# Optimization experiments

Hardware: AMD Instinct MI355X
Metric: run time of the kernel (lower is better)

Reference implementation:

```python
import jax, jax.numpy as jnp
import numpy as np

C_IN, C_OUT, K, PAD, STRIDE = 128, 256, 3, 1, 1
H = W = 256


def setup_inputs() -> dict:
    key = jax.random.key(0)
    k1, k2, k3 = jax.random.split(key, 3)
    # batch=1: the original forward uses X_pad[0] for every batch index,
    # so with m=1 the buggy loop and a standard conv are mathematically identical.
    x = jax.random.normal(k1, (1, C_IN, H, W), dtype=jnp.float32)
    # nn.Parameter(torch.rand(...)) -> uniform[0,1)
    weight = jax.random.uniform(k2, (C_OUT, C_IN, K, K), dtype=jnp.float32)
    bias = jax.random.uniform(k3, (C_OUT,), dtype=jnp.float32)
    return {"x": x, "weight": weight, "bias": bias}


def reference(x, weight, bias):
    # Faithful math of convAppx.forward with FP_appx_mul treated as exact
    # multiply (FP_appx_mul is not defined in the source): a plain 2D
    # cross-correlation (no kernel flip, matching the sliced elementwise
    # product) with symmetric padding, stride 1, plus per-channel bias.
    z = jax.lax.conv_general_dilated(
        x, weight,
        window_strides=(STRIDE, STRIDE),
        padding=((PAD, PAD), (PAD, PAD)),
        dimension_numbers=("NCHW", "OIHW", "NCHW"),
    )
    return z + bias[None, :, None, None]
```

## Files before the change

kernel.cpp:

```cpp
#include <hip/hip_runtime.h>
#include <hip/hip_bf16.h>


typedef short bf16x8 __attribute__((ext_vector_type(8)));
typedef float f32x4 __attribute__((ext_vector_type(4)));
typedef int   i32x4 __attribute__((ext_vector_type(4)));
typedef unsigned short u16x4 __attribute__((ext_vector_type(4)));
typedef unsigned short u16x8 __attribute__((ext_vector_type(8)));

#define CIN   128
#define COUT  256
#define HH    256
#define WW    256
#define HP    258
#define ROWP  (HP * CIN)

static __device__ __forceinline__ unsigned short f2bf(float v) {
    __hip_bfloat16 b = __float2bfloat16(v);
    return *reinterpret_cast<unsigned short*>(&b);
}

static __device__ __forceinline__ void gload_lds16(const unsigned short* g, unsigned short* l) {
    __builtin_amdgcn_global_load_lds(
        (const __attribute__((address_space(1))) unsigned int*)g,
        (__attribute__((address_space(3))) unsigned int*)l, 16, 0, 0);
}

template<int CTRL>
static __device__ __forceinline__ bf16x8 rotf(bf16x8 a) {
    i32x4 ai = __builtin_bit_cast(i32x4, a);
    i32x4 r;
    #pragma unroll
    for (int j = 0; j < 4; ++j)
        r[j] = __builtin_amdgcn_mov_dpp(ai[j], CTRL, 0xF, 0xF, true);
    return __builtin_bit_cast(bf16x8, r);
}
#define ROR_P1 0x12F
#define ROR_P2 0x12E

__global__ __launch_bounds__(256) void prep_kernel(const float* __restrict__ x,
                                                   const float* __restrict__ w,
                                                   unsigned short* __restrict__ xb,
                                                   unsigned short* __restrict__ wr) {
    int bid = blockIdx.x;
    int t   = threadIdx.x;

    if (bid < 65) {
        int i = bid * 256 + t;
        if (i < 16448) {
            u16x8 z = {0, 0, 0, 0, 0, 0, 0, 0};
            int off;
            if (i < 8256) {
                int r   = (i >= 4128) ? 1 : 0;
                int rem = i - r * 4128;
                off = (r * 257) * ROWP + rem * 8;
            } else {
                int j   = i - 8256;
                int col = j >> 12;
                int rem = j & 4095;
                int hp  = (rem >> 4) + 1;
                int c8  = rem & 15;
                off = hp * ROWP + (col * 257) * CIN + c8 * 8;
            }
            *(u16x8*)(&xb[off]) = z;
        }
    }

    if (bid < 128) {
        int p = bid * 256 + t;
        const float* src = w + p * 9;
        #pragma unroll
        for (int khw = 0; khw < 9; ++khw)
            wr[khw * (COUT * CIN) + p] = f2bf(src[khw]);
    }

    int h  = bid >> 2;
    int w0 = (bid & 3) * 64;
    __shared__ unsigned short tile[CIN * 72];

    int wq  = t & 15;
    int cib = t >> 4;
    for (int c0 = 0; c0 < CIN; c0 += 16) {
        int ci = c0 + cib;
        float4 v = *(const float4*)(x + ci * (HH * WW) + h * WW + w0 + wq * 4);
        u16x4 p;
        p.x = f2bf(v.x); p.y = f2bf(v.y); p.z = f2bf(v.z); p.w = f2bf(v.w);
        *(u16x4*)(&tile[ci * 72 + wq * 4]) = p;
    }
    __syncthreads();

    for (int it = 0; it < 4; ++it) {
        int idx = it * 256 + t;
        int ww_ = idx & 63;
        int c8  = idx >> 6;
        u16x8 o;
        #pragma unroll
        for (int j = 0; j < 8; ++j)
            o[j] = tile[(c8 * 8 + j) * 72 + ww_];
        int dst = ((h + 1) * HP + (w0 + ww_ + 1)) * CIN + c8 * 8;
        *(u16x8*)(&xb[dst]) = o;
    }
}

__global__ __launch_bounds__(512, 2) void conv_mfma_kernel(const unsigned short* __restrict__ xb,
                                                           const unsigned short* __restrict__ wr,
                                                           const float* __restrict__ bias,
                                                           float* __restrict__ out) {
    __shared__ unsigned short A0[256 * 64];
    __shared__ unsigned short A1[256 * 64];
    __shared__ unsigned short A2[256 * 64];
    __shared__ unsigned short Bs[258 * 64];

    int bid = blockIdx.x;
    int h   = (bid & 7) * 32 + (bid >> 3);

    int t    = threadIdx.x;
    int lane = t & 63;
    int wave = t >> 6;
    int wm   = wave >> 1;
    int wn   = wave & 1;
    int quad = lane >> 4;
    int l16  = lane & 15;

    f32x4 acc[4][8];
    #pragma unroll
    for (int mi = 0; mi < 4; ++mi)
        #pragma unroll
        for (int ni = 0; ni < 8; ++ni)
            acc[mi][ni] = (f32x4){0.f, 0.f, 0.f, 0.f};

    unsigned short* const Ap[3] = {A0, A1, A2};

    #pragma unroll 1
    for (int i = 0; i < 6; ++i) {
        int kh     = i >> 1;
        int cihalf = i & 1;

        #pragma unroll
        for (int p = 0; p < 3; ++p) {
            const unsigned short* wsrc = wr + (size_t)(kh * 3 + p) * (COUT * CIN) + cihalf * 64;
            unsigned short* dst = Ap[p];
            #pragma unroll
            for (int it = 0; it < 4; ++it) {
                int seg = it * 512 + t;
                int r   = seg >> 3;
                int s   = seg & 7;
                int c   = s ^ (r & 7);
                gload_lds16(wsrc + r * CIN + c * 8, &dst[seg * 8]);
            }
        }
        {
            const unsigned short* xrow = xb + (size_t)(h + kh) * ROWP + cihalf * 64;
            #pragma unroll
            for (int it = 0; it < 4; ++it) {
                int seg = it * 512 + t;
                int col = seg >> 3;
                int s   = seg & 7;
                int c   = s ^ (col & 7);
                gload_lds16(xrow + col * CIN + c * 8, &Bs[col * 64 + s * 8]);
            }
            if (t < 16) {
                int seg = 2048 + t;
                int col = seg >> 3;
                int s   = seg & 7;
                int c   = s ^ (col & 7);
                gload_lds16(xrow + col * CIN + c * 8, &Bs[col * 64 + s * 8]);
            }
        }
        asm volatile("s_waitcnt vmcnt(0)" ::: "memory");
        __builtin_amdgcn_s_barrier();
        __builtin_amdgcn_sched_barrier(0);

        #pragma unroll
        for (int kk = 0; kk < 2; ++kk) {
            int ck  = kk * 4 + quad;
            int asl = (ck ^ (l16 & 7)) * 8;

            bf16x8 af0[4], af1[4], af2[4];
            #pragma unroll
            for (int mi = 0; mi < 4; ++mi) {
                int ro = (wm * 64 + mi * 16 + l16) * 64;
                af0[mi] = *(const bf16x8*)(&A0[ro + asl]);
                af1[mi] = *(const bf16x8*)(&A1[ro + asl]);
                af2[mi] = *(const bf16x8*)(&A2[ro + asl]);
            }

            auto rdB = [&](int ni_) -> bf16x8 {
                int col = wn * 128 + ni_ * 16 + l16;
                if (col > 257) col = 257;
                return *(const bf16x8*)(&Bs[col * 64 + ((ck ^ (col & 7)) * 8)]);
            };

            bf16x8 cur = rdB(0);
            #pragma unroll
            for (int ni = 0; ni < 8; ++ni) {
                bf16x8 nxt = rdB(ni + 1);
                bf16x8 r1c = rotf<ROR_P1>(cur), r1n = rotf<ROR_P1>(nxt);
                bf16x8 s1  = (l16 == 15) ? r1n : r1c;
                bf16x8 r2c = rotf<ROR_P2>(cur), r2n = rotf<ROR_P2>(nxt);
                bf16x8 s2  = (l16 >= 14) ? r2n : r2c;

                __builtin_amdgcn_s_setprio(1);
                #pragma unroll
                for (int mi = 0; mi < 4; ++mi)
                    acc[mi][ni] = __builtin_amdgcn_mfma_f32_16x16x32_bf16(
                        af0[mi], cur, acc[mi][ni], 0, 0, 0);
                #pragma unroll
                for (int mi = 0; mi < 4; ++mi)
                    acc[mi][ni] = __builtin_amdgcn_mfma_f32_16x16x32_bf16(
                        af1[mi], s1, acc[mi][ni], 0, 0, 0);
                #pragma unroll
                for (int mi = 0; mi < 4; ++mi)
                    acc[mi][ni] = __builtin_amdgcn_mfma_f32_16x16x32_bf16(
                        af2[mi], s2, acc[mi][ni], 0, 0, 0);
                __builtin_amdgcn_s_setprio(0);
                cur = nxt;
            }
        }
        __builtin_amdgcn_s_barrier();
        __builtin_amdgcn_sched_barrier(0);
    }

    int sp0 = wn * 128 + l16;
    #pragma unroll
    for (int mi = 0; mi < 4; ++mi) {
        #pragma unroll
        for (int r = 0; r < 4; ++r) {
            int co = wm * 64 + mi * 16 + quad * 4 + r;
            float b = bias[co];
            float* orow = out + (size_t)co * (HH * WW) + h * WW + sp0;
            #pragma unroll
            for (int ni = 0; ni < 8; ++ni)
                orow[ni * 16] = acc[mi][ni][r] + b;
        }
    }
}

extern "C" void kernel_launch(void* const* d_in, const int* in_sizes, int n_in,
                              void* d_out, int out_size, void* d_ws, size_t ws_size,
                              hipStream_t stream) {
    const float* x    = (const float*)d_in[0];
    const float* w    = (const float*)d_in[1];
    const float* bias = (const float*)d_in[2];
    float* out        = (float*)d_out;

    unsigned short* xb = (unsigned short*)d_ws;
    unsigned short* wr = xb + (size_t)HP * HP * CIN;

    prep_kernel<<<dim3(1024), dim3(256), 0, stream>>>(x, w, xb, wr);
    conv_mfma_kernel<<<dim3(256), dim3(512), 0, stream>>>(xb, wr, bias, out);
}
```

Measured before the change: 136.9 us.

## Split conv blocks across output-channel halves and zero-pad edge columns in registers

Each block now handles one output row and a 128-channel half of the output channels, using 256 threads, and the grid doubles to 512 blocks. The LDS footprint shrinks (A tiles halve, and B holds only the 256 interior columns). Padding columns are no longer loaded but replaced with zeros at fragment-read time. This aims for better occupancy and CU coverage on a 256-CU part, at the cost of loading each input row twice, once per channel half, plus extra select logic in the B reads.

```diff
diff --git a/kernel.cpp b/kernel.cpp
--- a/kernel.cpp
+++ b/kernel.cpp
@@ -102,17 +102,19 @@
     }
 }
 
-__global__ __launch_bounds__(512, 2) void conv_mfma_kernel(const unsigned short* __restrict__ xb,
+__global__ __launch_bounds__(256, 2) void conv_mfma_kernel(const unsigned short* __restrict__ xb,
                                                            const unsigned short* __restrict__ wr,
                                                            const float* __restrict__ bias,
                                                            float* __restrict__ out) {
-    __shared__ unsigned short A0[256 * 64];
-    __shared__ unsigned short A1[256 * 64];
-    __shared__ unsigned short A2[256 * 64];
-    __shared__ unsigned short Bs[258 * 64];
-
-    int bid = blockIdx.x;
-    int h   = (bid & 7) * 32 + (bid >> 3);
+    __shared__ unsigned short A0[128 * 64];
+    __shared__ unsigned short A1[128 * 64];
+    __shared__ unsigned short A2[128 * 64];
+    __shared__ unsigned short Bs[256 * 64];
+
+    int bid   = blockIdx.x;
+    int inner = bid >> 3;
+    int h     = (bid & 7) * 32 + (inner >> 1);
+    int co0   = (inner & 1) * 128;
 
     int t    = threadIdx.x;
     int lane = t & 63;
@@ -138,11 +140,12 @@
 
         #pragma unroll
         for (int p = 0; p < 3; ++p) {
-            const unsigned short* wsrc = wr + (size_t)(kh * 3 + p) * (COUT * CIN) + cihalf * 64;
+            const unsigned short* wsrc =
+                wr + (size_t)(kh * 3 + p) * (COUT * CIN) + co0 * CIN + cihalf * 64;
             unsigned short* dst = Ap[p];
             #pragma unroll
             for (int it = 0; it < 4; ++it) {
-                int seg = it * 512 + t;
+                int seg = it * 256 + t;
                 int r   = seg >> 3;
                 int s   = seg & 7;
                 int c   = s ^ (r & 7);
@@ -152,19 +155,12 @@
         {
             const unsigned short* xrow = xb + (size_t)(h + kh) * ROWP + cihalf * 64;
             #pragma unroll
-            for (int it = 0; it < 4; ++it) {
-                int seg = it * 512 + t;
-                int col = seg >> 3;
+            for (int it = 0; it < 8; ++it) {
+                int seg = it * 256 + t;
+                int sc  = seg >> 3;
                 int s   = seg & 7;
-                int c   = s ^ (col & 7);
-                gload_lds16(xrow + col * CIN + c * 8, &Bs[col * 64 + s * 8]);
-            }
-            if (t < 16) {
-                int seg = 2048 + t;
-                int col = seg >> 3;
-                int s   = seg & 7;
-                int c   = s ^ (col & 7);
-                gload_lds16(xrow + col * CIN + c * 8, &Bs[col * 64 + s * 8]);
+                int c   = s ^ (sc & 7);
+                gload_lds16(xrow + (sc + 1) * CIN + c * 8, &Bs[seg * 8]);
             }
         }
         asm volatile("s_waitcnt vmcnt(0)" ::: "memory");
@@ -186,9 +182,15 @@
             }
 
             auto rdB = [&](int ni_) -> bf16x8 {
-                int col = wn * 128 + ni_ * 16 + l16;
-                if (col > 257) col = 257;
-                return *(const bf16x8*)(&Bs[col * 64 + ((ck ^ (col & 7)) * 8)]);
+                int pc  = wn * 128 + ni_ * 16 + l16;
+                int sc  = pc - 1;
+                int scc = sc < 0 ? 0 : (sc > 255 ? 255 : sc);
+                bf16x8 v = *(const bf16x8*)(&Bs[scc * 64 + ((ck ^ (scc & 7)) * 8)]);
+                if (pc < 1 || pc > 256) {
+                    bf16x8 z = {0, 0, 0, 0, 0, 0, 0, 0};
+                    v = z;
+                }
+                return v;
             };
 
             bf16x8 cur = rdB(0);
@@ -226,7 +228,7 @@
     for (int mi = 0; mi < 4; ++mi) {
         #pragma unroll
         for (int r = 0; r < 4; ++r) {
-            int co = wm * 64 + mi * 16 + quad * 4 + r;
+            int co = co0 + wm * 64 + mi * 16 + quad * 4 + r;
             float b = bias[co];
             float* orow = out + (size_t)co * (HH * WW) + h * WW + sp0;
             #pragma unroll
@@ -248,5 +250,5 @@
     unsigned short* wr = xb + (size_t)HP * HP * CIN;
 
     prep_kernel<<<dim3(1024), dim3(256), 0, stream>>>(x, w, xb, wr);
-    conv_mfma_kernel<<<dim3(256), dim3(512), 0, stream>>>(xb, wr, bias, out);
-}
+    conv_mfma_kernel<<<dim3(512), dim3(256), 0, stream>>>(xb, wr, bias, out);
+}
```

Result: slower. 144.6 us (+5.6%).
